# Performance work log

Measured on AMD Instinct MI355X. Metric: run time of the kernel, lower is better.

## Reference

```python
import jax, jax.numpy as jnp
import numpy as np

WIN = (8, 7, 7)
NUM_HEADS = 4
DIM = 128


def _part_xy(x, wh, ww):
    B, D, H, W, C = x.shape
    x = x.reshape(B, D, H // wh, wh, W // ww, ww, C).transpose(0, 1, 2, 4, 3, 5, 6)
    return x.reshape(-1, wh * ww, C)


def _rev_xy(win, wh, ww, D, Hp, Wp):
    C = win.shape[-1]
    x = win.reshape(-1, D, Hp // wh, Wp // ww, wh, ww, C).transpose(0, 1, 2, 4, 3, 5, 6)
    return x.reshape(-1, D, Hp, Wp, C)


def _part_ty(x, wd, wh):
    B, D, H, W, C = x.shape
    x = x.reshape(B, D // wd, wd, H // wh, wh, W, C).transpose(0, 1, 3, 5, 2, 4, 6)
    return x.reshape(-1, wd * wh, C)


def _rev_ty(win, wd, wh, Dp, Hp, W):
    C = win.shape[-1]
    x = win.reshape(-1, Dp // wd, Hp // wh, W, wd, wh, C).transpose(0, 1, 4, 2, 5, 3, 6)
    return x.reshape(-1, Dp, Hp, W, C)


def _part_tx(x, wd, ww):
    B, D, H, W, C = x.shape
    x = x.reshape(B, D // wd, wd, H, W // ww, ww, C).transpose(0, 1, 3, 4, 2, 5, 6)
    return x.reshape(-1, wd * ww, C)


def _rev_tx(win, wd, ww, Dp, H, Wp):
    C = win.shape[-1]
    x = win.reshape(-1, Dp // wd, H, Wp // ww, wd, ww, C).transpose(0, 1, 4, 2, 3, 5, 6)
    return x.reshape(-1, Dp, H, Wp, C)


def _attention(qkv):
    # qkv: [nw, n, 3*C] -> [3, nw, heads, n, head_c]
    nw, n, _ = qkv.shape
    head_c = DIM // NUM_HEADS
    scale = head_c ** -0.5
    qkv = qkv.reshape(nw, n, 3, NUM_HEADS, head_c).transpose(2, 0, 3, 1, 4)
    q, k, v = qkv[0] * scale, qkv[1], qkv[2]
    attn = jax.nn.softmax(jnp.einsum('whnc,whmc->whnm', q, k), axis=-1)
    out = jnp.einsum('whnm,whmc->whnc', attn, v)
    return out.transpose(0, 2, 1, 3).reshape(nw, n, DIM)


def setup_inputs() -> dict:
    key = jax.random.key(0)
    ks = jax.random.split(key, 8)
    B, D, H, W = 8, 8, 56, 56
    inp = {
        'x': jax.random.normal(ks[0], (B, D * H * W, DIM), jnp.float32),
        'qkv_w': jax.random.normal(ks[1], (DIM, 3 * DIM), jnp.float32) * 0.02,
        'qkv_b': jnp.zeros((3 * DIM,), jnp.float32),
        'qkv_th_w': jax.random.normal(ks[2], (DIM, 3 * DIM), jnp.float32) * 0.02,
        'qkv_th_b': jnp.zeros((3 * DIM,), jnp.float32),
        'qkv_tw_w': jax.random.normal(ks[3], (DIM, 3 * DIM), jnp.float32) * 0.02,
        'qkv_tw_b': jnp.zeros((3 * DIM,), jnp.float32),
        'proj_w': jax.random.normal(ks[4], (DIM, DIM), jnp.float32) * 0.02,
        'proj_b': jnp.zeros((DIM,), jnp.float32),
        'proj_th_w': jax.random.normal(ks[5], (DIM, DIM), jnp.float32) * 0.02,
        'proj_th_b': jnp.zeros((DIM,), jnp.float32),
        'proj_tw_w': jax.random.normal(ks[6], (DIM, DIM), jnp.float32) * 0.02,
        'proj_tw_b': jnp.zeros((DIM,), jnp.float32),
        'D': D, 'H': H, 'W': W,
    }
    return inp


def reference(x, qkv_w, qkv_b, qkv_th_w, qkv_th_b, qkv_tw_w, qkv_tw_b,
              proj_w, proj_b, proj_th_w, proj_th_b, proj_tw_w, proj_tw_b,
              D, H, W):
    wd, wh, ww = WIN
    B, N, C = x.shape
    x5 = x.reshape(B, D, H, W, C)
    pad_d1 = (-D) % wd
    pad_b = (-H) % wh
    pad_r = (-W) % ww
    # xy: pad H,W ; ty: pad D,H ; tx: pad D,W
    x_xy = jnp.pad(x5, ((0, 0), (0, 0), (0, pad_b), (0, pad_r), (0, 0)))
    x_th = jnp.pad(x5, ((0, 0), (0, pad_d1), (0, pad_b), (0, 0), (0, 0)))
    x_tw = jnp.pad(x5, ((0, 0), (0, pad_d1), (0, 0), (0, pad_r), (0, 0)))
    Hp, Wp = H + pad_b, W + pad_r
    Dp = D + pad_d1

    w_xy = _part_xy(x_xy, wh, ww)
    w_th = _part_ty(x_th, wd, wh)
    w_tw = _part_tx(x_tw, wd, ww)

    o_xy = _attention(w_xy @ qkv_w + qkv_b) @ proj_w + proj_b
    o_th = _attention(w_th @ qkv_th_w + qkv_th_b) @ proj_th_w + proj_th_b
    o_tw = _attention(w_tw @ qkv_tw_w + qkv_tw_b) @ proj_tw_w + proj_tw_b

    o_xy = _rev_xy(o_xy, wh, ww, D, Hp, Wp)[:, :, :H, :W, :]
    o_th = _rev_ty(o_th, wd, wh, Dp, Hp, W)[:, :D, :H, :, :]
    o_tw = _rev_tx(o_tw, wd, ww, Dp, H, Wp)[:, :D, :, :W, :]

    out = o_xy + o_th + o_tw
    return out.reshape(B, N, C)
```

## Files before the change

### kernel.cpp

```cpp
#include <hip/hip_runtime.h>


typedef __attribute__((ext_vector_type(8))) short short8v;
typedef __attribute__((ext_vector_type(4))) short short4v;
typedef __attribute__((ext_vector_type(4))) float floatx4;

#define MFMA16(a, b, c) __builtin_amdgcn_mfma_f32_16x16x32_bf16((a), (b), (c), 0, 0, 0)

#define SWZ8(row, b)  ((b) ^ (((row) & 7) << 4))
#define SWZ16(row, b) ((b) ^ (((row) & 15) << 4))

__device__ __forceinline__ short f2bf(float f) {
  unsigned u = __float_as_uint(f);
  u += 0x7fffu + ((u >> 16) & 1u);
  return (short)(u >> 16);
}

#define RA 0
#define RB 16384
#define RC 32768
#define LDS_BYTES 49152

template<int BRANCH>
__device__ __forceinline__ int win_base(int wid) {
  if constexpr (BRANCH == 0) {
    int b = wid >> 9, r = wid & 511;
    int d = r >> 6, hb = (r >> 3) & 7, wb = r & 7;
    return ((b * 8 + d) * 56 + hb * 7) * 56 + wb * 7;
  } else if constexpr (BRANCH == 1) {
    int b = wid / 448, r = wid % 448;
    int hb = r / 56, wc = r % 56;
    return (b * 8 * 56 + hb * 7) * 56 + wc;
  } else {
    int b = wid / 448, r = wid % 448;
    int h = r >> 3, wb = r & 7;
    return (b * 8 * 56 + h) * 56 + wb * 7;
  }
}
template<int BRANCH>
__device__ __forceinline__ int tok_off(int t) {
  int q = t / 7, rm = t - q * 7;
  if constexpr (BRANCH == 0) return q * 56 + rm;
  else if constexpr (BRANCH == 1) return q * 3136 + rm * 56;
  else return q * 3136 + rm;
}

__global__ void prep_weights(const float* __restrict__ q0, const float* __restrict__ q1,
                             const float* __restrict__ q2, const float* __restrict__ p0,
                             const float* __restrict__ p1, const float* __restrict__ p2,
                             short* __restrict__ ws) {
  int idx = blockIdx.x * 256 + threadIdx.x;
  if (idx < 3 * 49152) {
    int b = idx / 49152, r = idx % 49152;
    int n = r >> 7, k = r & 127;
    const float* s = (b == 0) ? q0 : (b == 1) ? q1 : q2;
    ws[idx] = f2bf(s[k * 384 + n]);
  } else if (idx < 3 * 49152 + 3 * 16384) {
    int j = idx - 3 * 49152;
    int b = j / 16384, r = j % 16384;
    int n = r >> 7, k = r & 127;
    const float* s = (b == 0) ? p0 : (b == 1) ? p1 : p2;
    ws[idx] = f2bf(s[k * 128 + n]);
  }
}

template<int BRANCH, int NTOK>
__global__ __launch_bounds__(512, 6)
void wattn(const float* __restrict__ x, const short* __restrict__ wqkvT,
           const float* __restrict__ bqkv, const short* __restrict__ wprojT,
           const float* __restrict__ bproj, float* __restrict__ out) {
  __shared__ alignas(256) char smem[LDS_BYTES];
  const int tid = threadIdx.x;
  const int w = tid >> 6;
  const int l = tid & 63;
  const int l15 = l & 15;
  const int l4 = l >> 4;
  const int base = win_base<BRANCH>(blockIdx.x);
  const float SCALE = 0.17677669529663687f;
  const floatx4 ZERO4 = {0.f, 0.f, 0.f, 0.f};

  {
    int rg = tid >> 5;
    int c4 = (tid & 31) << 2;
    #pragma unroll
    for (int it = 0; it < 4; ++it) {
      int t = rg + it * 16;
      short4v v4;
      if (t < NTOK) {
        float4 xv = *(const float4*)(x + (((size_t)(base + tok_off<BRANCH>(t))) << 7) + c4);
        v4.x = f2bf(xv.x); v4.y = f2bf(xv.y); v4.z = f2bf(xv.z); v4.w = f2bf(xv.w);
      } else {
        v4.x = 0; v4.y = 0; v4.z = 0; v4.w = 0;
      }
      *(short4v*)(&smem[RA + t * 256 + SWZ16(t, c4 * 2)]) = v4;
    }
  }
  __syncthreads();

  const int mt = w & 3, ng = w >> 2;
  const int arow = mt * 16 + l15;

  floatx4 vacc[4];
  {
    #pragma unroll
    for (int p = 0; p < 2; ++p) {
      floatx4 acc[4];
      #pragma unroll
      for (int i = 0; i < 4; ++i) acc[i] = ZERO4;
      #pragma unroll
      for (int kt = 0; kt < 4; ++kt) {
        short8v af = *(const short8v*)(&smem[RA + arow * 256 + SWZ16(arow, kt * 64 + l4 * 16)]);
        #pragma unroll
        for (int i = 0; i < 4; ++i) {
          int gcol = (p * 8 + ng * 4 + i) * 16 + l15;
          short8v bf = *(const short8v*)(wqkvT + (size_t)gcol * 128 + kt * 32 + l4 * 8);
          acc[i] = MFMA16(af, bf, acc[i]);
        }
      }
      int rbase = (p == 0) ? RB : RC;
      #pragma unroll
      for (int i = 0; i < 4; ++i) {
        int gcol = (p * 8 + ng * 4 + i) * 16 + l15;
        float bias = bqkv[gcol];
        int c = gcol - p * 128;
        #pragma unroll
        for (int r = 0; r < 4; ++r) {
          int row = mt * 16 + l4 * 4 + r;
          float v = acc[i][r] + bias;
          if (p == 0) v *= SCALE;
          *(short*)(&smem[rbase + row * 256 + SWZ16(row, c * 2)]) = f2bf(v);
        }
      }
    }
    #pragma unroll
    for (int i = 0; i < 4; ++i) vacc[i] = ZERO4;
    #pragma unroll
    for (int kt = 0; kt < 4; ++kt) {
      short8v af = *(const short8v*)(&smem[RA + arow * 256 + SWZ16(arow, kt * 64 + l4 * 16)]);
      #pragma unroll
      for (int i = 0; i < 4; ++i) {
        int gcol = (16 + ng * 4 + i) * 16 + l15;
        short8v bf = *(const short8v*)(wqkvT + (size_t)gcol * 128 + kt * 32 + l4 * 8);
        vacc[i] = MFMA16(af, bf, vacc[i]);
      }
    }
  }
  __syncthreads();

  {
    #pragma unroll
    for (int i = 0; i < 4; ++i) {
      int gcol = (16 + ng * 4 + i) * 16 + l15;
      float bias = bqkv[gcol];
      int c = gcol - 256;
      int kvb = mt * 16 + l4 * 4;
      short4v pv;
      #pragma unroll
      for (int r = 0; r < 4; ++r) pv[r] = f2bf(vacc[i][r] + bias);
      *(short4v*)(&smem[RA + c * 128 + SWZ8(c, kvb * 2)]) = pv;
    }
  }

  floatx4 ps[2][4];
  #pragma unroll
  for (int s2 = 0; s2 < 2; ++s2) {
    int s = w + s2 * 8;
    int h = s >> 2, smt = s & 3;
    int qrow = smt * 16 + l15;
    short8v aq = *(const short8v*)(&smem[RB + qrow * 256 + SWZ16(qrow, h * 64 + l4 * 16)]);
    floatx4 sa[4];
    #pragma unroll
    for (int nt = 0; nt < 4; ++nt) {
      int krow = nt * 16 + l15;
      short8v bk = *(const short8v*)(&smem[RC + krow * 256 + SWZ16(krow, h * 64 + l4 * 16)]);
      sa[nt] = MFMA16(aq, bk, ZERO4);
    }
    #pragma unroll
    for (int r = 0; r < 4; ++r) {
      float m0 = -1e30f;
      #pragma unroll
      for (int nt = 0; nt < 4; ++nt) {
        float sv = ((nt * 16 + l15) < NTOK) ? sa[nt][r] : -1e30f;
        sa[nt][r] = sv;
        m0 = fmaxf(m0, sv);
      }
      #pragma unroll
      for (int off = 1; off < 16; off <<= 1) m0 = fmaxf(m0, __shfl_xor(m0, off, 64));
      float sum = 0.f;
      #pragma unroll
      for (int nt = 0; nt < 4; ++nt) {
        float e = __expf(sa[nt][r] - m0);
        sa[nt][r] = e;
        sum += e;
      }
      #pragma unroll
      for (int off = 1; off < 16; off <<= 1) sum += __shfl_xor(sum, off, 64);
      float rs = __frcp_rn(sum);
      #pragma unroll
      for (int nt = 0; nt < 4; ++nt) ps[s2][nt][r] = sa[nt][r] * rs;
    }
  }
  __syncthreads();

  #pragma unroll
  for (int s2 = 0; s2 < 2; ++s2) {
    int s = w + s2 * 8;
    int h = s >> 2, smt = s & 3;
    int pb = RB + h * 8192;
    #pragma unroll
    for (int nt = 0; nt < 4; ++nt) {
      int col = nt * 16 + l15;
      #pragma unroll
      for (int r = 0; r < 4; ++r) {
        int row = smt * 16 + l4 * 4 + r;
        *(short*)(&smem[pb + row * 128 + SWZ8(row, col * 2)]) = f2bf(ps[s2][nt][r]);
      }
    }
  }
  __syncthreads();

  floatx4 oacc[4];
  {
    #pragma unroll
    for (int i = 0; i < 4; ++i) {
      int nt = ng * 4 + i;
      int h = nt >> 1;
      int pb = RB + h * 8192;
      int prow = mt * 16 + l15;
      int vrow = nt * 16 + l15;
      floatx4 a = ZERO4;
      #pragma unroll
      for (int kt = 0; kt < 2; ++kt) {
        short8v ap = *(const short8v*)(&smem[pb + prow * 128 + SWZ8(prow, kt * 64 + l4 * 16)]);
        short8v bv = *(const short8v*)(&smem[RA + vrow * 128 + SWZ8(vrow, kt * 64 + l4 * 16)]);
        a = MFMA16(ap, bv, a);
      }
      oacc[i] = a;
    }
  }
  __syncthreads();

  #pragma unroll
  for (int i = 0; i < 4; ++i) {
    int c = (ng * 4 + i) * 16 + l15;
    #pragma unroll
    for (int r = 0; r < 4; ++r) {
      int row = mt * 16 + l4 * 4 + r;
      *(short*)(&smem[RA + row * 256 + SWZ16(row, c * 2)]) = f2bf(oacc[i][r]);
    }
  }
  __syncthreads();

  {
    floatx4 pacc[4];
    #pragma unroll
    for (int i = 0; i < 4; ++i) pacc[i] = ZERO4;
    #pragma unroll
    for (int kt = 0; kt < 4; ++kt) {
      short8v ao = *(const short8v*)(&smem[RA + arow * 256 + SWZ16(arow, kt * 64 + l4 * 16)]);
      #pragma unroll
      for (int i = 0; i < 4; ++i) {
        int col = (ng * 4 + i) * 16 + l15;
        short8v bp = *(const short8v*)(wprojT + (size_t)col * 128 + kt * 32 + l4 * 8);
        pacc[i] = MFMA16(ao, bp, pacc[i]);
      }
    }
    #pragma unroll
    for (int i = 0; i < 4; ++i) {
      int col = (ng * 4 + i) * 16 + l15;
      float pb2 = bproj[col];
      #pragma unroll
      for (int r = 0; r < 4; ++r) {
        int row = mt * 16 + l4 * 4 + r;
        if (row < NTOK) {
          size_t gi = (((size_t)(base + tok_off<BRANCH>(row))) << 7) + col;
          if constexpr (BRANCH == 0) out[gi] = pacc[i][r] + pb2;
          else out[gi] += pacc[i][r] + pb2;
        }
      }
    }
  }
}

extern "C" void kernel_launch(void* const* d_in, const int* in_sizes, int n_in,
                              void* d_out, int out_size, void* d_ws, size_t ws_size,
                              hipStream_t stream) {
  const float* x         = (const float*)d_in[0];
  const float* qkv_w     = (const float*)d_in[1];
  const float* qkv_b     = (const float*)d_in[2];
  const float* qkv_th_w  = (const float*)d_in[3];
  const float* qkv_th_b  = (const float*)d_in[4];
  const float* qkv_tw_w  = (const float*)d_in[5];
  const float* qkv_tw_b  = (const float*)d_in[6];
  const float* proj_w    = (const float*)d_in[7];
  const float* proj_b    = (const float*)d_in[8];
  const float* proj_th_w = (const float*)d_in[9];
  const float* proj_th_b = (const float*)d_in[10];
  const float* proj_tw_w = (const float*)d_in[11];
  const float* proj_tw_b = (const float*)d_in[12];
  float* out = (float*)d_out;

  const int B = in_sizes[0] / (8 * 56 * 56 * 128);
  short* wsT = (short*)d_ws;

  prep_weights<<<768, 256, 0, stream>>>(qkv_w, qkv_th_w, qkv_tw_w,
                                        proj_w, proj_th_w, proj_tw_w, wsT);

  const short* qT0 = wsT;
  const short* qT1 = wsT + 49152;
  const short* qT2 = wsT + 2 * 49152;
  const short* pT0 = wsT + 3 * 49152;
  const short* pT1 = pT0 + 16384;
  const short* pT2 = pT0 + 2 * 16384;

  wattn<0, 49><<<B * 512, 512, 0, stream>>>(x, qT0, qkv_b,    pT0, proj_b,    out);
  wattn<1, 56><<<B * 448, 512, 0, stream>>>(x, qT1, qkv_th_b, pT1, proj_th_b, out);
  wattn<2, 56><<<B * 448, 512, 0, stream>>>(x, qT2, qkv_tw_b, pT2, proj_tw_b, out);
}
```

Measured before the change: 985.7 us.

## Merge three branch kernels into one launch with atomic accumulation and transposed scores

Replaces the three per-branch attention launches with a single kernel whose blocks pick their branch from the block index, so the grid has no tail gaps between launches. Output is now zeroed with a memset and accumulated with float atomicAdd, which removes the ordering dependency between branches. The QK^T product is computed transposed so each lane's softmax reduction needs only two cross-lane shuffles, and the probability tile is written with vector stores. The cost is an extra memset pass, atomic traffic on every output element, branch indices computed at runtime instead of as template constants, and a fast reciprocal in place of the correctly rounded one.

```diff
diff --git a/kernel.cpp b/kernel.cpp
--- a/kernel.cpp
+++ b/kernel.cpp
@@ -20,30 +20,6 @@
 #define RB 16384
 #define RC 32768
 #define LDS_BYTES 49152
-
-template<int BRANCH>
-__device__ __forceinline__ int win_base(int wid) {
-  if constexpr (BRANCH == 0) {
-    int b = wid >> 9, r = wid & 511;
-    int d = r >> 6, hb = (r >> 3) & 7, wb = r & 7;
-    return ((b * 8 + d) * 56 + hb * 7) * 56 + wb * 7;
-  } else if constexpr (BRANCH == 1) {
-    int b = wid / 448, r = wid % 448;
-    int hb = r / 56, wc = r % 56;
-    return (b * 8 * 56 + hb * 7) * 56 + wc;
-  } else {
-    int b = wid / 448, r = wid % 448;
-    int h = r >> 3, wb = r & 7;
-    return (b * 8 * 56 + h) * 56 + wb * 7;
-  }
-}
-template<int BRANCH>
-__device__ __forceinline__ int tok_off(int t) {
-  int q = t / 7, rm = t - q * 7;
-  if constexpr (BRANCH == 0) return q * 56 + rm;
-  else if constexpr (BRANCH == 1) return q * 3136 + rm * 56;
-  else return q * 3136 + rm;
-}
 
 __global__ void prep_weights(const float* __restrict__ q0, const float* __restrict__ q1,
                              const float* __restrict__ q2, const float* __restrict__ p0,
@@ -64,20 +40,45 @@
   }
 }
 
-template<int BRANCH, int NTOK>
 __global__ __launch_bounds__(512, 6)
-void wattn(const float* __restrict__ x, const short* __restrict__ wqkvT,
-           const float* __restrict__ bqkv, const short* __restrict__ wprojT,
-           const float* __restrict__ bproj, float* __restrict__ out) {
+void wattn_all(const float* __restrict__ x, const short* __restrict__ wsT,
+               const float* __restrict__ bq0, const float* __restrict__ bq1,
+               const float* __restrict__ bq2, const float* __restrict__ bp0,
+               const float* __restrict__ bp1, const float* __restrict__ bp2,
+               float* __restrict__ out, int nb0, int nb1) {
   __shared__ alignas(256) char smem[LDS_BYTES];
   const int tid = threadIdx.x;
   const int w = tid >> 6;
   const int l = tid & 63;
   const int l15 = l & 15;
   const int l4 = l >> 4;
-  const int base = win_base<BRANCH>(blockIdx.x);
   const float SCALE = 0.17677669529663687f;
   const floatx4 ZERO4 = {0.f, 0.f, 0.f, 0.f};
+
+  const int bid = blockIdx.x;
+  const int br = (bid >= nb0) + (bid >= nb0 + nb1);
+  const int lbid = bid - (br == 0 ? 0 : (br == 1 ? nb0 : nb0 + nb1));
+  const int NTOK = (br == 0) ? 49 : 56;
+  const int S1 = (br == 0) ? 56 : 3136;
+  const int S2 = (br == 1) ? 56 : 1;
+  int base;
+  if (br == 0) {
+    int b = lbid >> 9, r = lbid & 511;
+    int d = r >> 6, hb = (r >> 3) & 7, wb = r & 7;
+    base = ((b * 8 + d) * 56 + hb * 7) * 56 + wb * 7;
+  } else if (br == 1) {
+    int b = lbid / 448, r = lbid % 448;
+    int hb = r / 56, wc = r % 56;
+    base = (b * 448 + hb * 7) * 56 + wc;
+  } else {
+    int b = lbid / 448, r = lbid % 448;
+    int h = r >> 3, wb = r & 7;
+    base = (b * 448 + h) * 56 + wb * 7;
+  }
+  const short* wqkvT  = wsT + br * 49152;
+  const short* wprojT = wsT + 3 * 49152 + br * 16384;
+  const float* bqkv  = (br == 0) ? bq0 : (br == 1) ? bq1 : bq2;
+  const float* bproj = (br == 0) ? bp0 : (br == 1) ? bp1 : bp2;
 
   {
     int rg = tid >> 5;
@@ -87,7 +88,8 @@
       int t = rg + it * 16;
       short4v v4;
       if (t < NTOK) {
-        float4 xv = *(const float4*)(x + (((size_t)(base + tok_off<BRANCH>(t))) << 7) + c4);
+        int q = (unsigned)t / 7u, rm = t - q * 7;
+        float4 xv = *(const float4*)(x + (((size_t)(base + q * S1 + rm * S2)) << 7) + c4);
         v4.x = f2bf(xv.x); v4.y = f2bf(xv.y); v4.z = f2bf(xv.z); v4.w = f2bf(xv.w);
       } else {
         v4.x = 0; v4.y = 0; v4.z = 0; v4.w = 0;
@@ -161,43 +163,50 @@
     }
   }
 
-  floatx4 ps[2][4];
+  floatx4 pT[2][4];
   #pragma unroll
   for (int s2 = 0; s2 < 2; ++s2) {
     int s = w + s2 * 8;
-    int h = s >> 2, smt = s & 3;
-    int qrow = smt * 16 + l15;
-    short8v aq = *(const short8v*)(&smem[RB + qrow * 256 + SWZ16(qrow, h * 64 + l4 * 16)]);
-    floatx4 sa[4];
-    #pragma unroll
-    for (int nt = 0; nt < 4; ++nt) {
-      int krow = nt * 16 + l15;
-      short8v bk = *(const short8v*)(&smem[RC + krow * 256 + SWZ16(krow, h * 64 + l4 * 16)]);
-      sa[nt] = MFMA16(aq, bk, ZERO4);
-    }
-    #pragma unroll
-    for (int r = 0; r < 4; ++r) {
-      float m0 = -1e30f;
-      #pragma unroll
-      for (int nt = 0; nt < 4; ++nt) {
-        float sv = ((nt * 16 + l15) < NTOK) ? sa[nt][r] : -1e30f;
-        sa[nt][r] = sv;
+    int h = s >> 2, qt = s & 3;
+    int qrow = qt * 16 + l15;
+    short8v bq = *(const short8v*)(&smem[RB + qrow * 256 + SWZ16(qrow, h * 64 + l4 * 16)]);
+    floatx4 st[4];
+    #pragma unroll
+    for (int kvt = 0; kvt < 4; ++kvt) {
+      int krow = kvt * 16 + l15;
+      short8v ak = *(const short8v*)(&smem[RC + krow * 256 + SWZ16(krow, h * 64 + l4 * 16)]);
+      st[kvt] = MFMA16(ak, bq, ZERO4);
+    }
+    float m0 = -1e30f;
+    #pragma unroll
+    for (int kvt = 0; kvt < 4; ++kvt) {
+      #pragma unroll
+      for (int r = 0; r < 4; ++r) {
+        int kv = kvt * 16 + l4 * 4 + r;
+        float sv = (kv < NTOK) ? st[kvt][r] : -1e30f;
+        st[kvt][r] = sv;
         m0 = fmaxf(m0, sv);
       }
-      #pragma unroll
-      for (int off = 1; off < 16; off <<= 1) m0 = fmaxf(m0, __shfl_xor(m0, off, 64));
-      float sum = 0.f;
-      #pragma unroll
-      for (int nt = 0; nt < 4; ++nt) {
-        float e = __expf(sa[nt][r] - m0);
-        sa[nt][r] = e;
+    }
+    m0 = fmaxf(m0, __shfl_xor(m0, 16, 64));
+    m0 = fmaxf(m0, __shfl_xor(m0, 32, 64));
+    float sum = 0.f;
+    #pragma unroll
+    for (int kvt = 0; kvt < 4; ++kvt) {
+      #pragma unroll
+      for (int r = 0; r < 4; ++r) {
+        float e = __expf(st[kvt][r] - m0);
+        st[kvt][r] = e;
         sum += e;
       }
-      #pragma unroll
-      for (int off = 1; off < 16; off <<= 1) sum += __shfl_xor(sum, off, 64);
-      float rs = __frcp_rn(sum);
-      #pragma unroll
-      for (int nt = 0; nt < 4; ++nt) ps[s2][nt][r] = sa[nt][r] * rs;
+    }
+    sum += __shfl_xor(sum, 16, 64);
+    sum += __shfl_xor(sum, 32, 64);
+    float rs = __builtin_amdgcn_rcpf(sum);
+    #pragma unroll
+    for (int kvt = 0; kvt < 4; ++kvt) {
+      #pragma unroll
+      for (int r = 0; r < 4; ++r) pT[s2][kvt][r] = st[kvt][r] * rs;
     }
   }
   __syncthreads();
@@ -205,16 +214,15 @@
   #pragma unroll
   for (int s2 = 0; s2 < 2; ++s2) {
     int s = w + s2 * 8;
-    int h = s >> 2, smt = s & 3;
+    int h = s >> 2, qt = s & 3;
     int pb = RB + h * 8192;
-    #pragma unroll
-    for (int nt = 0; nt < 4; ++nt) {
-      int col = nt * 16 + l15;
-      #pragma unroll
-      for (int r = 0; r < 4; ++r) {
-        int row = smt * 16 + l4 * 4 + r;
-        *(short*)(&smem[pb + row * 128 + SWZ8(row, col * 2)]) = f2bf(ps[s2][nt][r]);
-      }
+    int qrow = qt * 16 + l15;
+    #pragma unroll
+    for (int kvt = 0; kvt < 4; ++kvt) {
+      short4v pw;
+      #pragma unroll
+      for (int r = 0; r < 4; ++r) pw[r] = f2bf(pT[s2][kvt][r]);
+      *(short4v*)(&smem[pb + qrow * 128 + SWZ8(qrow, kvt * 32 + l4 * 8)]) = pw;
     }
   }
   __syncthreads();
@@ -273,9 +281,9 @@
       for (int r = 0; r < 4; ++r) {
         int row = mt * 16 + l4 * 4 + r;
         if (row < NTOK) {
-          size_t gi = (((size_t)(base + tok_off<BRANCH>(row))) << 7) + col;
-          if constexpr (BRANCH == 0) out[gi] = pacc[i][r] + pb2;
-          else out[gi] += pacc[i][r] + pb2;
+          int q = (unsigned)row / 7u, rm = row - q * 7;
+          size_t gi = (((size_t)(base + q * S1 + rm * S2)) << 7) + col;
+          atomicAdd(&out[gi], pacc[i][r] + pb2);
         }
       }
     }
@@ -303,17 +311,12 @@
   const int B = in_sizes[0] / (8 * 56 * 56 * 128);
   short* wsT = (short*)d_ws;
 
+  hipMemsetAsync(d_out, 0, (size_t)out_size * sizeof(float), stream);
   prep_weights<<<768, 256, 0, stream>>>(qkv_w, qkv_th_w, qkv_tw_w,
                                         proj_w, proj_th_w, proj_tw_w, wsT);
 
-  const short* qT0 = wsT;
-  const short* qT1 = wsT + 49152;
-  const short* qT2 = wsT + 2 * 49152;
-  const short* pT0 = wsT + 3 * 49152;
-  const short* pT1 = pT0 + 16384;
-  const short* pT2 = pT0 + 2 * 16384;
-
-  wattn<0, 49><<<B * 512, 512, 0, stream>>>(x, qT0, qkv_b,    pT0, proj_b,    out);
-  wattn<1, 56><<<B * 448, 512, 0, stream>>>(x, qT1, qkv_th_b, pT1, proj_th_b, out);
-  wattn<2, 56><<<B * 448, 512, 0, stream>>>(x, qT2, qkv_tw_b, pT2, proj_tw_b, out);
+  const int nb0 = B * 512, nb1 = B * 448;
+  wattn_all<<<nb0 + 2 * nb1, 512, 0, stream>>>(
+      x, wsT, qkv_b, qkv_th_b, qkv_tw_b, proj_b, proj_th_b, proj_tw_b,
+      out, nb0, nb1);
 }
```

New measurement: 927.2 us. 1.06x faster.
